# Kernel tuning notes

Measured on AMD Instinct MI355X. Metric: run time of the kernel, lower is better.

## Reference

```python
import jax, jax.numpy as jnp
import numpy as np

N, E = 50000, 400000
IN_CH, HID, HEADS, EDGE_DIM = 128, 64, 4, 3
NEG_SLOPE = 0.2


def gatv2_conv(x, src, dst, edge_attr, Wl, Wr, We, att, bias):
    # x: [N, F_in]; Wl/Wr: [H*C, F_in]; We: [H*C, edge_dim]; att: [H, C]; bias: [C]
    H, C = att.shape
    n = x.shape[0]
    xl = (x @ Wl.T).reshape(n, H, C)   # source-side transform (lin_l)
    xr = (x @ Wr.T).reshape(n, H, C)   # target-side transform (lin_r)
    e = (edge_attr @ We.T).reshape(-1, H, C)
    z = jax.nn.leaky_relu(xl[src] + xr[dst] + e, NEG_SLOPE)  # [E,H,C]
    alpha = jnp.einsum('ehc,hc->eh', z, att)                 # [E,H]
    # segment softmax over incoming edges per destination node
    amax = jax.ops.segment_max(alpha, dst, num_segments=n)
    alpha = jnp.exp(alpha - amax[dst])
    denom = jax.ops.segment_sum(alpha, dst, num_segments=n)
    alpha = alpha / (denom[dst] + 1e-16)
    msg = xl[src] * alpha[:, :, None]                        # [E,H,C]
    out = jax.ops.segment_sum(msg, dst, num_segments=n)      # [N,H,C]
    return out.mean(axis=1) + bias                           # concat=False -> head mean


def setup_inputs() -> dict:
    key = jax.random.key(0)
    ks = jax.random.split(key, 16)
    s = 0.1
    return {
        'x': jax.random.normal(ks[0], (N, IN_CH), jnp.float32),
        'edge_index': jax.random.randint(ks[1], (2, E), 0, N, jnp.int32),
        'edge_attr': jax.random.normal(ks[2], (E, EDGE_DIM), jnp.float32),
        'Wl1': jax.random.normal(ks[3], (HEADS * HID, IN_CH), jnp.float32) * s,
        'Wr1': jax.random.normal(ks[4], (HEADS * HID, IN_CH), jnp.float32) * s,
        'We1': jax.random.normal(ks[5], (HEADS * HID, EDGE_DIM), jnp.float32) * s,
        'att1': jax.random.normal(ks[6], (HEADS, HID), jnp.float32) * s,
        'b1': jnp.zeros((HID,), jnp.float32),
        'Wl2': jax.random.normal(ks[7], (HEADS * HID, HID), jnp.float32) * s,
        'Wr2': jax.random.normal(ks[8], (HEADS * HID, HID), jnp.float32) * s,
        'We2': jax.random.normal(ks[9], (HEADS * HID, EDGE_DIM), jnp.float32) * s,
        'att2': jax.random.normal(ks[10], (HEADS, HID), jnp.float32) * s,
        'b2': jnp.zeros((HID,), jnp.float32),
        'prelu_w': jnp.full((HID,), 0.25, jnp.float32),
    }


def reference(x, edge_index, edge_attr, Wl1, Wr1, We1, att1, b1, Wl2, Wr2, We2, att2, b2, prelu_w):
    src, dst = edge_index[0], edge_index[1]
    h = gatv2_conv(x, src, dst, edge_attr, Wl1, Wr1, We1, att1, b1)
    h = gatv2_conv(h, src, dst, edge_attr, Wl2, Wr2, We2, att2, b2)
    return jnp.where(h >= 0, h, prelu_w * h)  # PReLU, per-channel weight
```

## Files before the change

kernel.cpp:

```cpp
#include <hip/hip_runtime.h>
#include <hip/hip_bf16.h>

#define HC 256

typedef __attribute__((ext_vector_type(8))) short bf16x8;
typedef __attribute__((ext_vector_type(4))) float f32x4;
typedef __attribute__((ext_vector_type(2))) float f32x2;

__device__ __forceinline__ void gl_lds16(const void* g, void* l) {
  __builtin_amdgcn_global_load_lds(
      (const __attribute__((address_space(1))) unsigned int*)g,
      (__attribute__((address_space(3))) unsigned int*)l, 16, 0, 0);
}

__device__ __forceinline__ void cast_w_one(const float* Wl, const float* Wr,
                                           ushort* WT, int F, int idx) {
  int col = idx / F, f = idx - col * F;
  float v = (col < 256) ? Wl[col * F + f] : Wr[(col - 256) * F + f];
  __hip_bfloat16 h = __float2bfloat16(v);
  WT[(size_t)col * F + f] = *(ushort*)&h;
}

__global__ void k_weights_hist(const float* __restrict__ Wl1, const float* __restrict__ Wr1,
                               ushort* __restrict__ WT1, const float* __restrict__ Wl2,
                               const float* __restrict__ Wr2, ushort* __restrict__ WT2,
                               const int* __restrict__ ei, int* __restrict__ deg, int E_) {
  int idx = blockIdx.x * blockDim.x + threadIdx.x;
  const int t1 = 512 * 128, t2 = 512 * 64;
  if (idx < t1) {
    cast_w_one(Wl1, Wr1, WT1, 128, idx);
  } else if (idx < t1 + t2) {
    cast_w_one(Wl2, Wr2, WT2, 64, idx - t1);
  } else {
    int e = idx - t1 - t2;
    if (e < E_) atomicAdd(&deg[ei[E_ + e]], 1);
  }
}

template <int F>
__global__ __launch_bounds__(256) void gemm_mfma(const ushort* __restrict__ A,
                                                 const ushort* __restrict__ WT,
                                                 ushort* __restrict__ xlb,
                                                 ushort* __restrict__ xrb, int n_nodes) {
  constexpr int NSTEP = F / 64;
  constexpr int SM = 17408;
  __shared__ __align__(16) ushort smem[SM];
  const int tid = threadIdx.x;
  const int wv = tid >> 6, lane = tid & 63;
  const int m16 = lane & 15, quad = lane >> 4;
  const int col0 = blockIdx.x * 128;
  const int row0 = blockIdx.y * 128;
  const int wm = (wv >> 1) * 64, wn = (wv & 1) * 64;

  f32x4 acc[4][4];
#pragma unroll
  for (int i = 0; i < 4; ++i)
#pragma unroll
    for (int j = 0; j < 4; ++j) acc[i][j] = (f32x4){0.f, 0.f, 0.f, 0.f};

  ushort* As = smem;
  ushort* Bs = smem + 8192;

  auto load_step = [&](int s) {
    const int khat = s * 64;
#pragma unroll
    for (int t = 0; t < 4; ++t) {
      const int sl16 = tid + 256 * t;
      const int row = sl16 >> 3, sl = sl16 & 7;
      const int gch = sl ^ (row & 7);
      const int grow = row0 + row;
      if (grow < n_nodes)
        gl_lds16(A + (size_t)grow * F + khat + gch * 8, As + sl16 * 8);
      gl_lds16(WT + (size_t)(col0 + row) * F + khat + gch * 8, Bs + sl16 * 8);
    }
  };

  auto mfma_step = [&]() {
#pragma unroll
    for (int kh = 0; kh < 2; ++kh) {
      bf16x8 af[4], bf[4];
#pragma unroll
      for (int i = 0; i < 4; ++i) {
        const int row = wm + i * 16 + m16;
        const int slot = (kh * 4 + quad) ^ (row & 7);
        af[i] = *(bf16x8*)&As[row * 64 + slot * 8];
      }
#pragma unroll
      for (int j = 0; j < 4; ++j) {
        const int col = wn + j * 16 + m16;
        const int slot = (kh * 4 + quad) ^ (col & 7);
        bf[j] = *(bf16x8*)&Bs[col * 64 + slot * 8];
      }
#pragma unroll
      for (int i = 0; i < 4; ++i)
#pragma unroll
        for (int j = 0; j < 4; ++j)
          acc[i][j] =
              __builtin_amdgcn_mfma_f32_16x16x32_bf16(af[i], bf[j], acc[i][j], 0, 0, 0);
    }
  };

  load_step(0);
  __syncthreads();
  mfma_step();
  if (NSTEP > 1) {
    __syncthreads();
    load_step(1);
    __syncthreads();
    mfma_step();
  }

  __syncthreads();
  ushort* Ct = smem;
#pragma unroll
  for (int i = 0; i < 4; ++i) {
#pragma unroll
    for (int r = 0; r < 4; ++r) {
      const int row = wm + i * 16 + quad * 4 + r;
#pragma unroll
      for (int j = 0; j < 4; ++j) {
        __hip_bfloat16 h = __float2bfloat16(acc[i][j][r]);
        Ct[row * 136 + wn + j * 16 + m16] = *(ushort*)&h;
      }
    }
  }
  __syncthreads();
  const bool is_xl = (col0 < 256);
  ushort* dst = is_xl ? xlb : xrb;
  const int cb = is_xl ? col0 : (col0 - 256);
  const int chunk = tid & 15;
#pragma unroll
  for (int it = 0; it < 8; ++it) {
    const int row = (tid >> 4) + 16 * it;
    const int grow = row0 + row;
    int4 v = *(int4*)&Ct[row * 136 + chunk * 8];
    if (grow < n_nodes)
      *(int4*)(dst + (size_t)grow * 256 + cb + chunk * 8) = v;
  }
}

__global__ void k_scan_local(const int* __restrict__ deg, int* __restrict__ rowstart,
                             int* __restrict__ partial, int n) {
  __shared__ int a[256], b[256];
  const int t = threadIdx.x;
  const int i = blockIdx.x * 256 + t;
  const int v = (i < n) ? deg[i] : 0;
  a[t] = v;
  __syncthreads();
  int* cur = a;
  int* nxt = b;
  for (int off = 1; off < 256; off <<= 1) {
    int x = cur[t];
    if (t >= off) x += cur[t - off];
    nxt[t] = x;
    __syncthreads();
    int* tmp = cur; cur = nxt; nxt = tmp;
  }
  const int incl = cur[t];
  if (i < n) rowstart[i] = incl - v;
  if (t == 255) partial[blockIdx.x] = incl;
}

__global__ void k_scan_final(const int* __restrict__ partial, int nblk,
                             int* __restrict__ rowstart, int* __restrict__ cursor,
                             float4* __restrict__ sea, int n, int E_) {
  __shared__ int a[256], b[256];
  const int t = threadIdx.x;
  const int v = (t < nblk) ? partial[t] : 0;
  a[t] = v;
  __syncthreads();
  int* cur = a;
  int* nxt = b;
  for (int off = 1; off < 256; off <<= 1) {
    int x = cur[t];
    if (t >= off) x += cur[t - off];
    nxt[t] = x;
    __syncthreads();
    int* tmp = cur; cur = nxt; nxt = tmp;
  }
  const int boff = (blockIdx.x > 0) ? cur[blockIdx.x - 1] : 0;
  const int i = blockIdx.x * 256 + t;
  if (i < n) {
    int vv = rowstart[i] + boff;
    rowstart[i] = vv;
    cursor[i] = vv;
  }
  if (i == 0) rowstart[n] = E_;
  if (blockIdx.x == 0 && t < 8) sea[E_ + t] = make_float4(0.f, 0.f, 0.f, 0.f);
}

__global__ void k_prep(const float* __restrict__ x, ushort* __restrict__ A,
                       const int* __restrict__ ei, const float* __restrict__ ea,
                       int* __restrict__ cursor, float4* __restrict__ sea,
                       int n, int E_) {
  const int nx8 = n * 16;
  int idx = blockIdx.x * blockDim.x + threadIdx.x;
  if (idx < nx8) {
    const float4* xp = (const float4*)x + (size_t)idx * 2;
    float4 v0 = xp[0], v1 = xp[1];
    float vv[8] = {v0.x, v0.y, v0.z, v0.w, v1.x, v1.y, v1.z, v1.w};
    __align__(16) ushort hb[8];
#pragma unroll
    for (int j = 0; j < 8; ++j) {
      __hip_bfloat16 h = __float2bfloat16(vv[j]);
      hb[j] = *(ushort*)&h;
    }
    *(int4*)(A + (size_t)idx * 8) = *(int4*)hb;
  } else {
    int e = idx - nx8;
    if (e < E_) {
      int dst = ei[E_ + e];
      int pos = atomicAdd(&cursor[dst], 1);
      sea[pos] = make_float4(ea[e * 3], ea[e * 3 + 1], ea[e * 3 + 2],
                             __int_as_float(ei[e] << 9));
    }
  }
}

__device__ __forceinline__ float dpp_ror_add(float p) {
  p += __int_as_float(__builtin_amdgcn_update_dpp(
      0, __float_as_int(p), 0x128, 0xF, 0xF, true));
  p += __int_as_float(__builtin_amdgcn_update_dpp(
      0, __float_as_int(p), 0x124, 0xF, 0xF, true));
  p += __int_as_float(__builtin_amdgcn_update_dpp(
      0, __float_as_int(p), 0x122, 0xF, 0xF, true));
  p += __int_as_float(__builtin_amdgcn_update_dpp(
      0, __float_as_int(p), 0x121, 0xF, 0xF, true));
  return p;
}

__device__ __forceinline__ void edge_step(
    const ushort4& lu, const float4& eav, const f32x2* we0, const f32x2* we1,
    const f32x2* we2, const f32x2* at6, const f32x2* at4, const f32x2* xrl,
    f32x2& num01, f32x2& num23, float& den) {
  f32x2 lav0, lav1;
  lav0.x = __uint_as_float((unsigned)lu.x << 16);
  lav0.y = __uint_as_float((unsigned)lu.y << 16);
  lav1.x = __uint_as_float((unsigned)lu.z << 16);
  lav1.y = __uint_as_float((unsigned)lu.w << 16);
  f32x2 pv = {0.f, 0.f};
#pragma unroll
  for (int j = 0; j < 2; ++j) {
    f32x2 la = (j == 0) ? lav0 : lav1;
    f32x2 t = xrl[j] + we0[j] * eav.x;
    t = t + we1[j] * eav.y;
    t = t + we2[j] * eav.z;
    f32x2 s = t + la;
    f32x2 sa = {fabsf(s.x), fabsf(s.y)};
    pv = pv + at6[j] * s;
    pv = pv + at4[j] * sa;
  }
  float p = pv.x + pv.y;
  p = dpp_ror_add(p);
  const float w = exp2f(p);
  den += w;
  num01 = num01 + (f32x2){w, w} * lav0;
  num23 = num23 + (f32x2){w, w} * lav1;
}

template <int MODE>
__global__ __launch_bounds__(64) void fused_attn(
    const ushort* __restrict__ xlb, const ushort* __restrict__ xrb,
    const int* __restrict__ rowstart, const float4* __restrict__ sea,
    const float* __restrict__ We, const float* __restrict__ att,
    const float* __restrict__ bias, const float* __restrict__ pw,
    float* __restrict__ out, ushort* __restrict__ outs, int n, int chunk) {
  const int lane = threadIdx.x;
  const int d0 = blockIdx.x * chunk;
  if (d0 >= n) return;
  const int d1 = min(d0 + chunk, n);

  f32x2 we0[2], we1[2], we2[2], at6[2], at4[2];
  const float L2E = 1.4426950408889634f;
#pragma unroll
  for (int j = 0; j < 4; ++j) {
    int r = 4 * lane + j;
    ((float*)we0)[j] = We[r * 3 + 0];
    ((float*)we1)[j] = We[r * 3 + 1];
    ((float*)we2)[j] = We[r * 3 + 2];
    float a = att[r];
    ((float*)at6)[j] = a * (0.6f * L2E);
    ((float*)at4)[j] = a * (0.4f * L2E);
  }
  const float4 bias4 = ((const float4*)bias)[lane & 15];
  float4 pw4 = {0.f, 0.f, 0.f, 0.f};
  if (MODE == 1) pw4 = ((const float4*)pw)[lane & 15];
  const char* xlbB = (const char*)xlb;
  const unsigned lane8 = (unsigned)lane * 8u;

#define GAT(e_) (*(const ushort4*)(xlbB + ((unsigned)__float_as_int((e_).w) + lane8)))

  for (int d = d0; d < d1; ++d) {
    const ushort4 xu = ((const ushort4*)xrb)[(unsigned)(d * 64) + lane];
    f32x2 xrl[2];
    xrl[0].x = __uint_as_float((unsigned)xu.x << 16);
    xrl[0].y = __uint_as_float((unsigned)xu.y << 16);
    xrl[1].x = __uint_as_float((unsigned)xu.z << 16);
    xrl[1].y = __uint_as_float((unsigned)xu.w << 16);

    int pos = __builtin_amdgcn_readfirstlane(rowstart[d]);
    const int end = __builtin_amdgcn_readfirstlane(rowstart[d + 1]);
    f32x2 num01 = {0.f, 0.f}, num23 = {0.f, 0.f};
    float den = 0.f;

    if (pos < end) {
      float4 e0 = sea[pos], e1 = sea[pos + 1], e2 = sea[pos + 2], e3 = sea[pos + 3];
      ushort4 g0 = GAT(e0), g1 = GAT(e1), g2 = GAT(e2), g3 = GAT(e3);

      while (pos + 4 <= end) {
        ushort4 h0 = g0, h1 = g1, h2 = g2, h3 = g3;
        float4 f0 = e0, f1 = e1, f2 = e2, f3 = e3;
        if (pos + 4 < end) {
          f0 = sea[pos + 4];
          f1 = sea[pos + 5];
          f2 = sea[pos + 6];
          f3 = sea[pos + 7];
          h0 = GAT(f0); h1 = GAT(f1); h2 = GAT(f2); h3 = GAT(f3);
        }
        edge_step(g0, e0, we0, we1, we2, at6, at4, xrl, num01, num23, den);
        edge_step(g1, e1, we0, we1, we2, at6, at4, xrl, num01, num23, den);
        edge_step(g2, e2, we0, we1, we2, at6, at4, xrl, num01, num23, den);
        edge_step(g3, e3, we0, we1, we2, at6, at4, xrl, num01, num23, den);
        g0 = h0; g1 = h1; g2 = h2; g3 = h3;
        e0 = f0; e1 = f1; e2 = f2; e3 = f3;
        pos += 4;
      }
      const int rem = end - pos;
      if (rem > 0) edge_step(g0, e0, we0, we1, we2, at6, at4, xrl, num01, num23, den);
      if (rem > 1) edge_step(g1, e1, we0, we1, we2, at6, at4, xrl, num01, num23, den);
      if (rem > 2) edge_step(g2, e2, we0, we1, we2, at6, at4, xrl, num01, num23, den);
    }

    const float inv = 1.f / (den + 1e-16f);
    float4 r;
    r.x = num01.x * inv;
    r.y = num01.y * inv;
    r.z = num23.x * inv;
    r.w = num23.y * inv;
    r.x += __shfl_xor(r.x, 16);
    r.y += __shfl_xor(r.y, 16);
    r.z += __shfl_xor(r.z, 16);
    r.w += __shfl_xor(r.w, 16);
    r.x += __shfl_xor(r.x, 32);
    r.y += __shfl_xor(r.y, 32);
    r.z += __shfl_xor(r.z, 32);
    r.w += __shfl_xor(r.w, 32);
    if (lane < 16) {
      float o[4];
      o[0] = 0.25f * r.x + bias4.x;
      o[1] = 0.25f * r.y + bias4.y;
      o[2] = 0.25f * r.z + bias4.z;
      o[3] = 0.25f * r.w + bias4.w;
      if (MODE == 1) {
        const float pwv[4] = {pw4.x, pw4.y, pw4.z, pw4.w};
#pragma unroll
        for (int j = 0; j < 4; ++j) o[j] = (o[j] >= 0.f) ? o[j] : pwv[j] * o[j];
        ((float4*)out)[(size_t)d * 16 + lane] = make_float4(o[0], o[1], o[2], o[3]);
      } else {
        ushort hb[4];
#pragma unroll
        for (int j = 0; j < 4; ++j) {
          __hip_bfloat16 h = __float2bfloat16(o[j]);
          hb[j] = *(ushort*)&h;
        }
        *(ushort4*)(outs + (size_t)d * 64 + 4 * lane) =
            make_ushort4(hb[0], hb[1], hb[2], hb[3]);
      }
    }
  }
#undef GAT
}

extern "C" void kernel_launch(void* const* d_in, const int* in_sizes, int n_in,
                              void* d_out, int out_size, void* d_ws, size_t ws_size,
                              hipStream_t stream) {
  const float* x    = (const float*)d_in[0];
  const int*   ei   = (const int*)d_in[1];
  const float* ea   = (const float*)d_in[2];
  const float* Wl1  = (const float*)d_in[3];
  const float* Wr1  = (const float*)d_in[4];
  const float* We1  = (const float*)d_in[5];
  const float* att1 = (const float*)d_in[6];
  const float* b1   = (const float*)d_in[7];
  const float* Wl2  = (const float*)d_in[8];
  const float* Wr2  = (const float*)d_in[9];
  const float* We2  = (const float*)d_in[10];
  const float* att2 = (const float*)d_in[11];
  const float* b2   = (const float*)d_in[12];
  const float* pw   = (const float*)d_in[13];
  const int N_ = in_sizes[0] / 128;
  const int E_ = in_sizes[1] / 2;
  float* out = (float*)d_out;

  char* w = (char*)d_ws;
  auto alloc = [&](size_t bytes) {
    char* p = w;
    w += (bytes + 255) & ~size_t(255);
    return p;
  };
  ushort* xlb      = (ushort*)alloc((size_t)N_ * 256 * 2);
  ushort* xrb      = (ushort*)alloc((size_t)N_ * 256 * 2);
  ushort* Ax       = (ushort*)alloc((size_t)N_ * 128 * 2);
  ushort* h2       = (ushort*)alloc((size_t)N_ * 64 * 2);
  float4* sea      = (float4*)alloc((size_t)(E_ + 8) * 16);
  int*    deg      = (int*)alloc((size_t)N_ * 4);
  int*    rowstart = (int*)alloc((size_t)(N_ + 1) * 4);
  int*    cursor   = (int*)alloc((size_t)N_ * 4);
  int*    partial  = (int*)alloc(256 * 4);
  ushort* WT1      = (ushort*)alloc((size_t)512 * 128 * 2);
  ushort* WT2      = (ushort*)alloc((size_t)512 * 64 * 2);

  hipMemsetAsync(deg, 0, (size_t)N_ * 4, stream);
  const int wtot = 512 * 128 + 512 * 64 + E_;
  k_weights_hist<<<(wtot + 255) / 256, 256, 0, stream>>>(Wl1, Wr1, WT1, Wl2, Wr2, WT2,
                                                         ei, deg, E_);

  const int nblk = (N_ + 255) / 256;
  k_scan_local<<<nblk, 256, 0, stream>>>(deg, rowstart, partial, N_);
  k_scan_final<<<nblk, 256, 0, stream>>>(partial, nblk, rowstart, cursor, sea, N_, E_);
  const int ptot = N_ * 16 + E_;
  k_prep<<<(ptot + 255) / 256, 256, 0, stream>>>(x, Ax, ei, ea, cursor, sea, N_, E_);

  const dim3 GG(4, (N_ + 127) / 128);
  const int chunk = 2;
  const int FB = (N_ + chunk - 1) / chunk;

  gemm_mfma<128><<<GG, 256, 0, stream>>>(Ax, WT1, xlb, xrb, N_);
  fused_attn<0><<<FB, 64, 0, stream>>>(xlb, xrb, rowstart, sea, We1, att1,
                                       b1, pw, nullptr, h2, N_, chunk);
  gemm_mfma<64><<<GG, 256, 0, stream>>>(h2, WT2, xlb, xrb, N_);
  fused_attn<1><<<FB, 64, 0, stream>>>(xlb, xrb, rowstart, sea, We2, att2,
                                       b2, pw, out, nullptr, N_, chunk);
}
```

Baseline: 260.5 us.

## Use persistent blocks with atomic work-stealing for attention node scheduling

Replaces one 64-thread block per pair of destination nodes with a fixed grid of 4096 blocks of 128 threads. Each wavefront repeatedly grabs two nodes from a global atomic counter, which is zeroed in the scan kernel. This aims to cut launch and scheduling overhead for about 25k tiny blocks and to balance load across uneven node degrees. The cost is one atomic per two nodes, contended across many wavefronts.

```diff
diff --git a/kernel.cpp b/kernel.cpp
--- a/kernel.cpp
+++ b/kernel.cpp
@@ -163,7 +163,8 @@
 
 __global__ void k_scan_final(const int* __restrict__ partial, int nblk,
                              int* __restrict__ rowstart, int* __restrict__ cursor,
-                             float4* __restrict__ sea, int n, int E_) {
+                             float4* __restrict__ sea, int* __restrict__ wk,
+                             int n, int E_) {
   __shared__ int a[256], b[256];
   const int t = threadIdx.x;
   const int v = (t < nblk) ? partial[t] : 0;
@@ -187,6 +188,7 @@
   }
   if (i == 0) rowstart[n] = E_;
   if (blockIdx.x == 0 && t < 8) sea[E_ + t] = make_float4(0.f, 0.f, 0.f, 0.f);
+  if (blockIdx.x == 0 && t < 2) wk[t] = 0;
 }
 
 __global__ void k_prep(const float* __restrict__ x, ushort* __restrict__ A,
@@ -259,16 +261,14 @@
 }
 
 template <int MODE>
-__global__ __launch_bounds__(64) void fused_attn(
+__global__ __launch_bounds__(128) void fused_attn(
     const ushort* __restrict__ xlb, const ushort* __restrict__ xrb,
     const int* __restrict__ rowstart, const float4* __restrict__ sea,
     const float* __restrict__ We, const float* __restrict__ att,
     const float* __restrict__ bias, const float* __restrict__ pw,
-    float* __restrict__ out, ushort* __restrict__ outs, int n, int chunk) {
-  const int lane = threadIdx.x;
-  const int d0 = blockIdx.x * chunk;
-  if (d0 >= n) return;
-  const int d1 = min(d0 + chunk, n);
+    float* __restrict__ out, ushort* __restrict__ outs,
+    int* __restrict__ wkcur, int n, int chunk) {
+  const int lane = threadIdx.x & 63;
 
   f32x2 we0[2], we1[2], we2[2], at6[2], at4[2];
   const float L2E = 1.4426950408889634f;
@@ -290,81 +290,89 @@
 
 #define GAT(e_) (*(const ushort4*)(xlbB + ((unsigned)__float_as_int((e_).w) + lane8)))
 
-  for (int d = d0; d < d1; ++d) {
-    const ushort4 xu = ((const ushort4*)xrb)[(unsigned)(d * 64) + lane];
-    f32x2 xrl[2];
-    xrl[0].x = __uint_as_float((unsigned)xu.x << 16);
-    xrl[0].y = __uint_as_float((unsigned)xu.y << 16);
-    xrl[1].x = __uint_as_float((unsigned)xu.z << 16);
-    xrl[1].y = __uint_as_float((unsigned)xu.w << 16);
-
-    int pos = __builtin_amdgcn_readfirstlane(rowstart[d]);
-    const int end = __builtin_amdgcn_readfirstlane(rowstart[d + 1]);
-    f32x2 num01 = {0.f, 0.f}, num23 = {0.f, 0.f};
-    float den = 0.f;
-
-    if (pos < end) {
-      float4 e0 = sea[pos], e1 = sea[pos + 1], e2 = sea[pos + 2], e3 = sea[pos + 3];
-      ushort4 g0 = GAT(e0), g1 = GAT(e1), g2 = GAT(e2), g3 = GAT(e3);
-
-      while (pos + 4 <= end) {
-        ushort4 h0 = g0, h1 = g1, h2 = g2, h3 = g3;
-        float4 f0 = e0, f1 = e1, f2 = e2, f3 = e3;
-        if (pos + 4 < end) {
-          f0 = sea[pos + 4];
-          f1 = sea[pos + 5];
-          f2 = sea[pos + 6];
-          f3 = sea[pos + 7];
-          h0 = GAT(f0); h1 = GAT(f1); h2 = GAT(f2); h3 = GAT(f3);
+  for (;;) {
+    int base;
+    if (lane == 0) base = atomicAdd(wkcur, chunk);
+    base = __shfl(base, 0);
+    if (base >= n) break;
+    const int d1 = min(base + chunk, n);
+
+    for (int d = base; d < d1; ++d) {
+      const ushort4 xu = ((const ushort4*)xrb)[(unsigned)(d * 64) + lane];
+      f32x2 xrl[2];
+      xrl[0].x = __uint_as_float((unsigned)xu.x << 16);
+      xrl[0].y = __uint_as_float((unsigned)xu.y << 16);
+      xrl[1].x = __uint_as_float((unsigned)xu.z << 16);
+      xrl[1].y = __uint_as_float((unsigned)xu.w << 16);
+
+      int pos = __builtin_amdgcn_readfirstlane(rowstart[d]);
+      const int end = __builtin_amdgcn_readfirstlane(rowstart[d + 1]);
+      f32x2 num01 = {0.f, 0.f}, num23 = {0.f, 0.f};
+      float den = 0.f;
+
+      if (pos < end) {
+        float4 e0 = sea[pos], e1 = sea[pos + 1], e2 = sea[pos + 2], e3 = sea[pos + 3];
+        ushort4 g0 = GAT(e0), g1 = GAT(e1), g2 = GAT(e2), g3 = GAT(e3);
+
+        while (pos + 4 <= end) {
+          ushort4 h0 = g0, h1 = g1, h2 = g2, h3 = g3;
+          float4 f0 = e0, f1 = e1, f2 = e2, f3 = e3;
+          if (pos + 4 < end) {
+            f0 = sea[pos + 4];
+            f1 = sea[pos + 5];
+            f2 = sea[pos + 6];
+            f3 = sea[pos + 7];
+            h0 = GAT(f0); h1 = GAT(f1); h2 = GAT(f2); h3 = GAT(f3);
+          }
+          edge_step(g0, e0, we0, we1, we2, at6, at4, xrl, num01, num23, den);
+          edge_step(g1, e1, we0, we1, we2, at6, at4, xrl, num01, num23, den);
+          edge_step(g2, e2, we0, we1, we2, at6, at4, xrl, num01, num23, den);
+          edge_step(g3, e3, we0, we1, we2, at6, at4, xrl, num01, num23, den);
+          g0 = h0; g1 = h1; g2 = h2; g3 = h3;
+          e0 = f0; e1 = f1; e2 = f2; e3 = f3;
+          pos += 4;
         }
-        edge_step(g0, e0, we0, we1, we2, at6, at4, xrl, num01, num23, den);
-        edge_step(g1, e1, we0, we1, we2, at6, at4, xrl, num01, num23, den);
-        edge_step(g2, e2, we0, we1, we2, at6, at4, xrl, num01, num23, den);
-        edge_step(g3, e3, we0, we1, we2, at6, at4, xrl, num01, num23, den);
-        g0 = h0; g1 = h1; g2 = h2; g3 = h3;
-        e0 = f0; e1 = f1; e2 = f2; e3 = f3;
-        pos += 4;
+        const int rem = end - pos;
+        if (rem > 0) edge_step(g0, e0, we0, we1, we2, at6, at4, xrl, num01, num23, den);
+        if (rem > 1) edge_step(g1, e1, we0, we1, we2, at6, at4, xrl, num01, num23, den);
+        if (rem > 2) edge_step(g2, e2, we0, we1, we2, at6, at4, xrl, num01, num23, den);
       }
-      const int rem = end - pos;
-      if (rem > 0) edge_step(g0, e0, we0, we1, we2, at6, at4, xrl, num01, num23, den);
-      if (rem > 1) edge_step(g1, e1, we0, we1, we2, at6, at4, xrl, num01, num23, den);
-      if (rem > 2) edge_step(g2, e2, we0, we1, we2, at6, at4, xrl, num01, num23, den);
-    }
-
-    const float inv = 1.f / (den + 1e-16f);
-    float4 r;
-    r.x = num01.x * inv;
-    r.y = num01.y * inv;
-    r.z = num23.x * inv;
-    r.w = num23.y * inv;
-    r.x += __shfl_xor(r.x, 16);
-    r.y += __shfl_xor(r.y, 16);
-    r.z += __shfl_xor(r.z, 16);
-    r.w += __shfl_xor(r.w, 16);
-    r.x += __shfl_xor(r.x, 32);
-    r.y += __shfl_xor(r.y, 32);
-    r.z += __shfl_xor(r.z, 32);
-    r.w += __shfl_xor(r.w, 32);
-    if (lane < 16) {
-      float o[4];
-      o[0] = 0.25f * r.x + bias4.x;
-      o[1] = 0.25f * r.y + bias4.y;
-      o[2] = 0.25f * r.z + bias4.z;
-      o[3] = 0.25f * r.w + bias4.w;
-      if (MODE == 1) {
-        const float pwv[4] = {pw4.x, pw4.y, pw4.z, pw4.w};
-#pragma unroll
-        for (int j = 0; j < 4; ++j) o[j] = (o[j] >= 0.f) ? o[j] : pwv[j] * o[j];
-        ((float4*)out)[(size_t)d * 16 + lane] = make_float4(o[0], o[1], o[2], o[3]);
-      } else {
-        ushort hb[4];
-#pragma unroll
-        for (int j = 0; j < 4; ++j) {
-          __hip_bfloat16 h = __float2bfloat16(o[j]);
-          hb[j] = *(ushort*)&h;
+
+      const float inv = 1.f / (den + 1e-16f);
+      float4 r;
+      r.x = num01.x * inv;
+      r.y = num01.y * inv;
+      r.z = num23.x * inv;
+      r.w = num23.y * inv;
+      r.x += __shfl_xor(r.x, 16);
+      r.y += __shfl_xor(r.y, 16);
+      r.z += __shfl_xor(r.z, 16);
+      r.w += __shfl_xor(r.w, 16);
+      r.x += __shfl_xor(r.x, 32);
+      r.y += __shfl_xor(r.y, 32);
+      r.z += __shfl_xor(r.z, 32);
+      r.w += __shfl_xor(r.w, 32);
+      if (lane < 16) {
+        float o[4];
+        o[0] = 0.25f * r.x + bias4.x;
+        o[1] = 0.25f * r.y + bias4.y;
+        o[2] = 0.25f * r.z + bias4.z;
+        o[3] = 0.25f * r.w + bias4.w;
+        if (MODE == 1) {
+          const float pwv[4] = {pw4.x, pw4.y, pw4.z, pw4.w};
+#pragma unroll
+          for (int j = 0; j < 4; ++j) o[j] = (o[j] >= 0.f) ? o[j] : pwv[j] * o[j];
+          ((float4*)out)[(size_t)d * 16 + lane] = make_float4(o[0], o[1], o[2], o[3]);
+        } else {
+          ushort hb[4];
+#pragma unroll
+          for (int j = 0; j < 4; ++j) {
+            __hip_bfloat16 h = __float2bfloat16(o[j]);
+            hb[j] = *(ushort*)&h;
+          }
+          *(ushort4*)(outs + (size_t)d * 64 + 4 * lane) =
+              make_ushort4(hb[0], hb[1], hb[2], hb[3]);
         }
-        *(ushort4*)(outs + (size_t)d * 64 + 4 * lane) =
-            make_ushort4(hb[0], hb[1], hb[2], hb[3]);
       }
     }
   }
@@ -407,6 +415,7 @@
   int*    rowstart = (int*)alloc((size_t)(N_ + 1) * 4);
   int*    cursor   = (int*)alloc((size_t)N_ * 4);
   int*    partial  = (int*)alloc(256 * 4);
+  int*    wk       = (int*)alloc(8);
   ushort* WT1      = (ushort*)alloc((size_t)512 * 128 * 2);
   ushort* WT2      = (ushort*)alloc((size_t)512 * 64 * 2);
 
@@ -417,18 +426,18 @@
 
   const int nblk = (N_ + 255) / 256;
   k_scan_local<<<nblk, 256, 0, stream>>>(deg, rowstart, partial, N_);
-  k_scan_final<<<nblk, 256, 0, stream>>>(partial, nblk, rowstart, cursor, sea, N_, E_);
+  k_scan_final<<<nblk, 256, 0, stream>>>(partial, nblk, rowstart, cursor, sea, wk, N_, E_);
   const int ptot = N_ * 16 + E_;
   k_prep<<<(ptot + 255) / 256, 256, 0, stream>>>(x, Ax, ei, ea, cursor, sea, N_, E_);
 
   const dim3 GG(4, (N_ + 127) / 128);
   const int chunk = 2;
-  const int FB = (N_ + chunk - 1) / chunk;
+  const int FB = 4096;
 
   gemm_mfma<128><<<GG, 256, 0, stream>>>(Ax, WT1, xlb, xrb, N_);
-  fused_attn<0><<<FB, 64, 0, stream>>>(xlb, xrb, rowstart, sea, We1, att1,
-                                       b1, pw, nullptr, h2, N_, chunk);
+  fused_attn<0><<<FB, 128, 0, stream>>>(xlb, xrb, rowstart, sea, We1, att1,
+                                        b1, pw, nullptr, h2, wk + 0, N_, chunk);
   gemm_mfma<64><<<GG, 256, 0, stream>>>(h2, WT2, xlb, xrb, N_);
-  fused_attn<1><<<FB, 64, 0, stream>>>(xlb, xrb, rowstart, sea, We2, att2,
-                                       b2, pw, out, nullptr, N_, chunk);
-}
+  fused_attn<1><<<FB, 128, 0, stream>>>(xlb, xrb, rowstart, sea, We2, att2,
+                                        b2, pw, out, nullptr, wk + 1, N_, chunk);
+}
```

New measurement: 946.9 us. 3.64x slower.

## Fuse preprocessing kernels into one persistent kernel with grid-wide barriers

Applied to the files above, without the earlier changes.

Merges the weight cast, degree histogram, two-level scan, x-to-bf16 conversion and CSR edge scatter into a single 256-block persistent kernel. Stages are separated by atomic-counter grid barriers instead of separate launches, and one memset now clears both the barrier counters and the degree array. This is meant to remove launch gaps between small kernels. In exchange, 256 blocks must all be co-resident for the spin barriers to avoid deadlock, and the grid-stride loops use fewer threads than the original launches.

```diff
diff --git a/kernel.cpp b/kernel.cpp
--- a/kernel.cpp
+++ b/kernel.cpp
@@ -11,30 +11,6 @@
   __builtin_amdgcn_global_load_lds(
       (const __attribute__((address_space(1))) unsigned int*)g,
       (__attribute__((address_space(3))) unsigned int*)l, 16, 0, 0);
-}
-
-__device__ __forceinline__ void cast_w_one(const float* Wl, const float* Wr,
-                                           ushort* WT, int F, int idx) {
-  int col = idx / F, f = idx - col * F;
-  float v = (col < 256) ? Wl[col * F + f] : Wr[(col - 256) * F + f];
-  __hip_bfloat16 h = __float2bfloat16(v);
-  WT[(size_t)col * F + f] = *(ushort*)&h;
-}
-
-__global__ void k_weights_hist(const float* __restrict__ Wl1, const float* __restrict__ Wr1,
-                               ushort* __restrict__ WT1, const float* __restrict__ Wl2,
-                               const float* __restrict__ Wr2, ushort* __restrict__ WT2,
-                               const int* __restrict__ ei, int* __restrict__ deg, int E_) {
-  int idx = blockIdx.x * blockDim.x + threadIdx.x;
-  const int t1 = 512 * 128, t2 = 512 * 64;
-  if (idx < t1) {
-    cast_w_one(Wl1, Wr1, WT1, 128, idx);
-  } else if (idx < t1 + t2) {
-    cast_w_one(Wl2, Wr2, WT2, 64, idx - t1);
-  } else {
-    int e = idx - t1 - t2;
-    if (e < E_) atomicAdd(&deg[ei[E_ + e]], 1);
-  }
 }
 
 template <int F>
@@ -139,64 +115,47 @@
   }
 }
 
-__global__ void k_scan_local(const int* __restrict__ deg, int* __restrict__ rowstart,
-                             int* __restrict__ partial, int n) {
-  __shared__ int a[256], b[256];
+__device__ __forceinline__ void cast_w_one(const float* Wl, const float* Wr,
+                                           ushort* WT, int F, int idx) {
+  int col = idx / F, f = idx - col * F;
+  float v = (col < 256) ? Wl[col * F + f] : Wr[(col - 256) * F + f];
+  __hip_bfloat16 h = __float2bfloat16(v);
+  WT[(size_t)col * F + f] = *(ushort*)&h;
+}
+
+__device__ __forceinline__ void gsync(int* cnt, int nblk) {
+  __syncthreads();
+  if (threadIdx.x == 0) {
+    __threadfence();
+    atomicAdd(cnt, 1);
+    while (__hip_atomic_load(cnt, __ATOMIC_ACQUIRE, __HIP_MEMORY_SCOPE_AGENT) < nblk) {
+      __builtin_amdgcn_s_sleep(2);
+    }
+    __threadfence();
+  }
+  __syncthreads();
+}
+
+__global__ __launch_bounds__(256) void k_mega_prep(
+    const float* __restrict__ x, const int* __restrict__ ei,
+    const float* __restrict__ ea, const float* __restrict__ Wl1,
+    const float* __restrict__ Wr1, const float* __restrict__ Wl2,
+    const float* __restrict__ Wr2, ushort* __restrict__ Ax,
+    ushort* __restrict__ WT1, ushort* __restrict__ WT2, int* __restrict__ deg,
+    int* __restrict__ rowstart, int* __restrict__ cursor,
+    int* __restrict__ partial, float4* __restrict__ sea, int* __restrict__ cnts,
+    int n, int E_) {
+  __shared__ int a_[256], b_[256];
   const int t = threadIdx.x;
-  const int i = blockIdx.x * 256 + t;
-  const int v = (i < n) ? deg[i] : 0;
-  a[t] = v;
-  __syncthreads();
-  int* cur = a;
-  int* nxt = b;
-  for (int off = 1; off < 256; off <<= 1) {
-    int x = cur[t];
-    if (t >= off) x += cur[t - off];
-    nxt[t] = x;
-    __syncthreads();
-    int* tmp = cur; cur = nxt; nxt = tmp;
-  }
-  const int incl = cur[t];
-  if (i < n) rowstart[i] = incl - v;
-  if (t == 255) partial[blockIdx.x] = incl;
-}
-
-__global__ void k_scan_final(const int* __restrict__ partial, int nblk,
-                             int* __restrict__ rowstart, int* __restrict__ cursor,
-                             float4* __restrict__ sea, int n, int E_) {
-  __shared__ int a[256], b[256];
-  const int t = threadIdx.x;
-  const int v = (t < nblk) ? partial[t] : 0;
-  a[t] = v;
-  __syncthreads();
-  int* cur = a;
-  int* nxt = b;
-  for (int off = 1; off < 256; off <<= 1) {
-    int x = cur[t];
-    if (t >= off) x += cur[t - off];
-    nxt[t] = x;
-    __syncthreads();
-    int* tmp = cur; cur = nxt; nxt = tmp;
-  }
-  const int boff = (blockIdx.x > 0) ? cur[blockIdx.x - 1] : 0;
-  const int i = blockIdx.x * 256 + t;
-  if (i < n) {
-    int vv = rowstart[i] + boff;
-    rowstart[i] = vv;
-    cursor[i] = vv;
-  }
-  if (i == 0) rowstart[n] = E_;
-  if (blockIdx.x == 0 && t < 8) sea[E_ + t] = make_float4(0.f, 0.f, 0.f, 0.f);
-}
-
-__global__ void k_prep(const float* __restrict__ x, ushort* __restrict__ A,
-                       const int* __restrict__ ei, const float* __restrict__ ea,
-                       int* __restrict__ cursor, float4* __restrict__ sea,
-                       int n, int E_) {
-  const int nx8 = n * 16;
-  int idx = blockIdx.x * blockDim.x + threadIdx.x;
-  if (idx < nx8) {
-    const float4* xp = (const float4*)x + (size_t)idx * 2;
+  const int b = blockIdx.x;
+  const int tid = b * 256 + t;
+  const int T = 256 * 256;
+  const int nblk_scan = (n + 255) >> 8;
+
+  for (int i = tid; i < 512 * 128; i += T) cast_w_one(Wl1, Wr1, WT1, 128, i);
+  for (int i = tid; i < 512 * 64; i += T) cast_w_one(Wl2, Wr2, WT2, 64, i);
+  for (int i = tid; i < n * 16; i += T) {
+    const float4* xp = (const float4*)x + (size_t)i * 2;
     float4 v0 = xp[0], v1 = xp[1];
     float vv[8] = {v0.x, v0.y, v0.z, v0.w, v1.x, v1.y, v1.z, v1.w};
     __align__(16) ushort hb[8];
@@ -205,15 +164,61 @@
       __hip_bfloat16 h = __float2bfloat16(vv[j]);
       hb[j] = *(ushort*)&h;
     }
-    *(int4*)(A + (size_t)idx * 8) = *(int4*)hb;
-  } else {
-    int e = idx - nx8;
-    if (e < E_) {
-      int dst = ei[E_ + e];
-      int pos = atomicAdd(&cursor[dst], 1);
-      sea[pos] = make_float4(ea[e * 3], ea[e * 3 + 1], ea[e * 3 + 2],
-                             __int_as_float(ei[e] << 9));
-    }
+    *(int4*)(Ax + (size_t)i * 8) = *(int4*)hb;
+  }
+  for (int e = tid; e < E_; e += T) atomicAdd(&deg[ei[E_ + e]], 1);
+  if (tid < 8) sea[E_ + tid] = make_float4(0.f, 0.f, 0.f, 0.f);
+  gsync(cnts + 0, 256);
+
+  if (b < nblk_scan) {
+    const int i = b * 256 + t;
+    const int v = (i < n) ? deg[i] : 0;
+    a_[t] = v;
+    __syncthreads();
+    int* cur = a_;
+    int* nxt = b_;
+    for (int off = 1; off < 256; off <<= 1) {
+      int xv = cur[t];
+      if (t >= off) xv += cur[t - off];
+      nxt[t] = xv;
+      __syncthreads();
+      int* tmp = cur; cur = nxt; nxt = tmp;
+    }
+    const int incl = cur[t];
+    if (i < n) rowstart[i] = incl - v;
+    if (t == 255) partial[b] = incl;
+  }
+  gsync(cnts + 1, 256);
+
+  if (b < nblk_scan) {
+    const int v = (t < nblk_scan) ? partial[t] : 0;
+    a_[t] = v;
+    __syncthreads();
+    int* cur = a_;
+    int* nxt = b_;
+    for (int off = 1; off < 256; off <<= 1) {
+      int xv = cur[t];
+      if (t >= off) xv += cur[t - off];
+      nxt[t] = xv;
+      __syncthreads();
+      int* tmp = cur; cur = nxt; nxt = tmp;
+    }
+    const int boff = (b > 0) ? cur[b - 1] : 0;
+    const int i = b * 256 + t;
+    if (i < n) {
+      int vv = rowstart[i] + boff;
+      rowstart[i] = vv;
+      cursor[i] = vv;
+    }
+    if (b == 0 && t == 0) rowstart[n] = E_;
+  }
+  gsync(cnts + 2, 256);
+
+  for (int e = tid; e < E_; e += T) {
+    int dst = ei[E_ + e];
+    int pos = atomicAdd(&cursor[dst], 1);
+    sea[pos] = make_float4(ea[e * 3], ea[e * 3 + 1], ea[e * 3 + 2],
+                           __int_as_float(ei[e] << 9));
   }
 }
 
@@ -398,28 +403,24 @@
     w += (bytes + 255) & ~size_t(255);
     return p;
   };
+  int*    cnts     = (int*)alloc(256);
+  int*    deg      = (int*)alloc((size_t)N_ * 4);
   ushort* xlb      = (ushort*)alloc((size_t)N_ * 256 * 2);
   ushort* xrb      = (ushort*)alloc((size_t)N_ * 256 * 2);
   ushort* Ax       = (ushort*)alloc((size_t)N_ * 128 * 2);
   ushort* h2       = (ushort*)alloc((size_t)N_ * 64 * 2);
   float4* sea      = (float4*)alloc((size_t)(E_ + 8) * 16);
-  int*    deg      = (int*)alloc((size_t)N_ * 4);
   int*    rowstart = (int*)alloc((size_t)(N_ + 1) * 4);
   int*    cursor   = (int*)alloc((size_t)N_ * 4);
   int*    partial  = (int*)alloc(256 * 4);
   ushort* WT1      = (ushort*)alloc((size_t)512 * 128 * 2);
   ushort* WT2      = (ushort*)alloc((size_t)512 * 64 * 2);
 
-  hipMemsetAsync(deg, 0, (size_t)N_ * 4, stream);
-  const int wtot = 512 * 128 + 512 * 64 + E_;
-  k_weights_hist<<<(wtot + 255) / 256, 256, 0, stream>>>(Wl1, Wr1, WT1, Wl2, Wr2, WT2,
-                                                         ei, deg, E_);
-
-  const int nblk = (N_ + 255) / 256;
-  k_scan_local<<<nblk, 256, 0, stream>>>(deg, rowstart, partial, N_);
-  k_scan_final<<<nblk, 256, 0, stream>>>(partial, nblk, rowstart, cursor, sea, N_, E_);
-  const int ptot = N_ * 16 + E_;
-  k_prep<<<(ptot + 255) / 256, 256, 0, stream>>>(x, Ax, ei, ea, cursor, sea, N_, E_);
+  hipMemsetAsync(cnts, 0, 256 + (size_t)N_ * 4, stream);
+
+  k_mega_prep<<<256, 256, 0, stream>>>(x, ei, ea, Wl1, Wr1, Wl2, Wr2, Ax, WT1,
+                                       WT2, deg, rowstart, cursor, partial, sea,
+                                       cnts, N_, E_);
 
   const dim3 GG(4, (N_ + 127) / 128);
   const int chunk = 2;
```

Result: slower. 332.5 us (+27.7%).
